# Performance work log

Hardware: AMD Instinct MI355X
Metric: run time of the kernel (lower is better)

Reference implementation:

```python
import jax, jax.numpy as jnp
import numpy as np

B, G, FI, FO, H, W = 16, 8, 64, 64, 64, 64
N_ITER = 3


def setup_inputs() -> dict:
    key = jax.random.key(0)
    kx, kw, kb = jax.random.split(key, 3)
    x = jax.random.normal(kx, (B, G * FI, H, W), dtype=jnp.float32)
    # kaiming_normal_ on [fo*g, fi, 1, 1]: std = sqrt(2 / fan_in), fan_in = fi*1*1
    weight = jax.random.normal(kw, (FO * G, FI, 1, 1), dtype=jnp.float32) * np.sqrt(2.0 / FI)
    bias = jax.random.normal(kb, (1, FO, 1, 1), dtype=jnp.float32) * 0.01
    return {"x": x, "weight": weight, "bias": bias}


def reference(x, weight, bias):
    g, n_iter = G, N_ITER
    gfo, fi = weight.shape[:2]
    fo = gfo // g
    b, c, h, w = x.shape
    # grouped 1x1 conv == per-group channel matmul
    xg = x.reshape(b, g, fi, h, w)
    wg = weight.reshape(g, fo, fi)
    con = jnp.einsum('bgihw,gfi->bgfhw', xg, wg)  # [B, g, fo, H, W]
    beta = jnp.zeros((), dtype=x.dtype)
    for i in range(n_iter):
        alpha = jax.nn.sigmoid(beta)
        v = jnp.sum(alpha * con, axis=1, keepdims=True)  # [B, 1, fo, H, W]
        if i == n_iter - 1:
            out = v[:, 0]  # [B, fo, H, W]
            return out + bias
        beta = beta + jnp.sum(v * con, axis=2, keepdims=True)  # [B, g, 1, H, W]
```

## Files before the change

kernel.cpp:

```cpp
#include <hip/hip_runtime.h>


typedef __attribute__((ext_vector_type(8))) _Float16 half8;
typedef __attribute__((ext_vector_type(4))) float f32x4;

#define NG   8
#define NFI  64
#define NFO  64
#define HW   4096

__device__ __forceinline__ float sigmoidf_fast(float v) {
    float e = __builtin_amdgcn_exp2f(-1.44269504088896f * v);
    return __builtin_amdgcn_rcpf(1.0f + e);
}

__global__ __launch_bounds__(256)
void wconv_kernel(const float* __restrict__ w, _Float16* __restrict__ wbuf) {
    int V = blockIdx.x * 256 + threadIdx.x;
    int g    = V >> 10;
    int t    = (V >> 8) & 3;
    int c    = (V >> 6) & 3;
    int lane = V & 63;
    int pl = lane & 15, q = lane >> 4;
    const float* src = w + g * (NFO * NFI) + (t * 16 + pl) * NFI + (c & 1) * 32 + q * 8;
    half8 o;
    #pragma unroll
    for (int j = 0; j < 8; ++j) {
        float f = src[j];
        _Float16 h = (_Float16)f;
        o[j] = (c >> 1) ? (_Float16)(f - (float)h) : h;
    }
    *(half8*)(wbuf + (size_t)V * 8) = o;
}

__global__ __launch_bounds__(256, 2)
void routing_kernel(const float* __restrict__ x,
                    const _Float16* __restrict__ wbuf,
                    const float* __restrict__ bias,
                    float* __restrict__ out) {
    const int tid  = threadIdx.x;
    const int b    = blockIdx.x >> 6;
    const int p0   = (blockIdx.x & 63) << 6;
    const int lane = tid & 63;
    const int wv   = tid >> 6;
    const int pl   = lane & 15;
    const int q    = lane >> 4;
    const int pw   = wv * 16 + pl;

    const float* xg = x + (size_t)b * (NG * NFI) * HW + p0 + pw;

    f32x4 acc[NG][4];
    #pragma unroll
    for (int g = 0; g < NG; ++g)
        #pragma unroll
        for (int t = 0; t < 4; ++t)
            acc[g][t] = (f32x4){0.f, 0.f, 0.f, 0.f};

#define XDECL(NM) float NM##0, NM##1, NM##2, NM##3, NM##4, NM##5, NM##6, NM##7, \
                        NM##8, NM##9, NM##10, NM##11, NM##12, NM##13, NM##14, NM##15;
#define XLOAD(G, NM)                                                         \
    {                                                                        \
        const float* p_ = xg + (size_t)((G) * 64 + q * 8) * HW;              \
        NM##0 = p_[(size_t)0 * HW];  NM##1 = p_[(size_t)1 * HW];             \
        NM##2 = p_[(size_t)2 * HW];  NM##3 = p_[(size_t)3 * HW];             \
        NM##4 = p_[(size_t)4 * HW];  NM##5 = p_[(size_t)5 * HW];             \
        NM##6 = p_[(size_t)6 * HW];  NM##7 = p_[(size_t)7 * HW];             \
        const float* p2_ = p_ + (size_t)32 * HW;                             \
        NM##8  = p2_[(size_t)0 * HW]; NM##9  = p2_[(size_t)1 * HW];          \
        NM##10 = p2_[(size_t)2 * HW]; NM##11 = p2_[(size_t)3 * HW];          \
        NM##12 = p2_[(size_t)4 * HW]; NM##13 = p2_[(size_t)5 * HW];          \
        NM##14 = p2_[(size_t)6 * HW]; NM##15 = p2_[(size_t)7 * HW];          \
    }
#define XGRP(G, NM)                                                          \
    {                                                                        \
        half8 b0, b1;                                                        \
        b0[0] = (_Float16)NM##0;  b0[1] = (_Float16)NM##1;                   \
        b0[2] = (_Float16)NM##2;  b0[3] = (_Float16)NM##3;                   \
        b0[4] = (_Float16)NM##4;  b0[5] = (_Float16)NM##5;                   \
        b0[6] = (_Float16)NM##6;  b0[7] = (_Float16)NM##7;                   \
        b1[0] = (_Float16)NM##8;  b1[1] = (_Float16)NM##9;                   \
        b1[2] = (_Float16)NM##10; b1[3] = (_Float16)NM##11;                  \
        b1[4] = (_Float16)NM##12; b1[5] = (_Float16)NM##13;                  \
        b1[6] = (_Float16)NM##14; b1[7] = (_Float16)NM##15;                  \
        const _Float16* wg_ = wbuf + (size_t)(G) * 16 * 512 + lane * 8;      \
        _Pragma("unroll")                                                    \
        for (int t = 0; t < 4; ++t) {                                        \
            const _Float16* wp_ = wg_ + (size_t)t * 2048;                    \
            half8 a0h = *(const half8*)(wp_);                                \
            half8 a1h = *(const half8*)(wp_ + 512);                          \
            half8 a0l = *(const half8*)(wp_ + 1024);                         \
            half8 a1l = *(const half8*)(wp_ + 1536);                         \
            acc[G][t] = __builtin_amdgcn_mfma_f32_16x16x32_f16(a0h, b0, acc[G][t], 0, 0, 0); \
            acc[G][t] = __builtin_amdgcn_mfma_f32_16x16x32_f16(a1h, b1, acc[G][t], 0, 0, 0); \
            acc[G][t] = __builtin_amdgcn_mfma_f32_16x16x32_f16(a0l, b0, acc[G][t], 0, 0, 0); \
            acc[G][t] = __builtin_amdgcn_mfma_f32_16x16x32_f16(a1l, b1, acc[G][t], 0, 0, 0); \
        }                                                                    \
    }

    XDECL(X0) XDECL(X1) XDECL(X2)

    XLOAD(0, X0)
    XLOAD(1, X1)
    XLOAD(2, X2) XGRP(0, X0)
    XLOAD(3, X0) XGRP(1, X1)
    XLOAD(4, X1) XGRP(2, X2)
    XLOAD(5, X2) XGRP(3, X0)
    XLOAD(6, X0) XGRP(4, X1)
    XLOAD(7, X1) XGRP(5, X2)
    XGRP(6, X0)
    XGRP(7, X1)

#undef XDECL
#undef XLOAD
#undef XGRP

    float v0[4][4];
    #pragma unroll
    for (int t = 0; t < 4; ++t)
        #pragma unroll
        for (int r = 0; r < 4; ++r) {
            float s = 0.f;
            #pragma unroll
            for (int g = 0; g < NG; ++g) s += acc[g][t][r];
            v0[t][r] = 0.5f * s;
        }

    float beta[NG], alpha[NG];
    #pragma unroll
    for (int g = 0; g < NG; ++g) {
        float s = 0.f;
        #pragma unroll
        for (int t = 0; t < 4; ++t)
            #pragma unroll
            for (int r = 0; r < 4; ++r)
                s += v0[t][r] * acc[g][t][r];
        s += __shfl_xor(s, 16);
        s += __shfl_xor(s, 32);
        beta[g]  = s;
        alpha[g] = sigmoidf_fast(s);
    }

    #pragma unroll
    for (int t = 0; t < 4; ++t)
        #pragma unroll
        for (int r = 0; r < 4; ++r) {
            float s = 0.f;
            #pragma unroll
            for (int g = 0; g < NG; ++g) s += alpha[g] * acc[g][t][r];
            v0[t][r] = s;
        }
    #pragma unroll
    for (int g = 0; g < NG; ++g) {
        float s = 0.f;
        #pragma unroll
        for (int t = 0; t < 4; ++t)
            #pragma unroll
            for (int r = 0; r < 4; ++r)
                s += v0[t][r] * acc[g][t][r];
        s += __shfl_xor(s, 16);
        s += __shfl_xor(s, 32);
        beta[g] += s;
        alpha[g] = sigmoidf_fast(beta[g]);
    }

    #pragma unroll
    for (int t = 0; t < 4; ++t)
        #pragma unroll
        for (int r = 0; r < 4; ++r) {
            int f = t * 16 + q * 4 + r;
            float s = bias[f];
            #pragma unroll
            for (int g = 0; g < NG; ++g) s += alpha[g] * acc[g][t][r];
            out[((size_t)(b * NFO + f)) * HW + p0 + pw] = s;
        }
}

extern "C" void kernel_launch(void* const* d_in, const int* in_sizes, int n_in,
                              void* d_out, int out_size, void* d_ws, size_t ws_size,
                              hipStream_t stream) {
    const float* x    = (const float*)d_in[0];
    const float* w    = (const float*)d_in[1];
    const float* bias = (const float*)d_in[2];
    float* out = (float*)d_out;
    _Float16* wbuf = (_Float16*)d_ws;

    wconv_kernel<<<32, 256, 0, stream>>>(w, wbuf);
    routing_kernel<<<1024, 256, 0, stream>>>(x, wbuf, bias, out);
}
```

Before: 211.6 us.

## Stage per-group weights into LDS with double-buffered async global_load_lds

Instead of every wave reading the fp16 split weight fragments straight from global memory for each group, the block cooperatively copies each group's weights into a double-buffered LDS array using global_load_lds. The copies are interleaved with the x loads, with explicit vmcnt waits and barriers. This is meant to cut redundant global/L2 weight traffic across the four waves and overlap weight fetch with MFMA work. In exchange it adds 32KB of LDS per block, which may limit occupancy, plus block barriers per group and fragile hand-counted waitcnt values.

Result: faster. 206.2 us (-2.5%).

```diff
diff --git a/kernel.cpp b/kernel.cpp
--- a/kernel.cpp
+++ b/kernel.cpp
@@ -47,6 +47,8 @@
     const int q    = lane >> 4;
     const int pw   = wv * 16 + pl;
 
+    __shared__ _Float16 wlds[2][16 * 512];
+
     const float* xg = x + (size_t)b * (NG * NFI) * HW + p0 + pw;
 
     f32x4 acc[NG][4];
@@ -55,6 +57,29 @@
         #pragma unroll
         for (int t = 0; t < 4; ++t)
             acc[g][t] = (f32x4){0.f, 0.f, 0.f, 0.f};
+
+#define CB   asm volatile("" ::: "memory")
+#define BAR  __builtin_amdgcn_s_barrier()
+#define SB0  __builtin_amdgcn_sched_barrier(0)
+#define WAITV(N) asm volatile("s_waitcnt vmcnt(" #N ")" ::: "memory")
+
+#define WSTAGE(G, BUF)                                                        \
+    {                                                                         \
+        const _Float16* ws_ = wbuf + (size_t)(G) * 8192 + (wv * 4) * 512 + lane * 8; \
+        _Float16* wd_ = &wlds[BUF][0] + (wv * 4) * 512;                       \
+        __builtin_amdgcn_global_load_lds(                                     \
+            (const __attribute__((address_space(1))) void*)(ws_),             \
+            (__attribute__((address_space(3))) void*)(wd_), 16, 0, 0);        \
+        __builtin_amdgcn_global_load_lds(                                     \
+            (const __attribute__((address_space(1))) void*)(ws_ + 512),       \
+            (__attribute__((address_space(3))) void*)(wd_ + 512), 16, 0, 0);  \
+        __builtin_amdgcn_global_load_lds(                                     \
+            (const __attribute__((address_space(1))) void*)(ws_ + 1024),      \
+            (__attribute__((address_space(3))) void*)(wd_ + 1024), 16, 0, 0); \
+        __builtin_amdgcn_global_load_lds(                                     \
+            (const __attribute__((address_space(1))) void*)(ws_ + 1536),      \
+            (__attribute__((address_space(3))) void*)(wd_ + 1536), 16, 0, 0); \
+    }
 
 #define XDECL(NM) float NM##0, NM##1, NM##2, NM##3, NM##4, NM##5, NM##6, NM##7, \
                         NM##8, NM##9, NM##10, NM##11, NM##12, NM##13, NM##14, NM##15;
@@ -71,7 +96,7 @@
         NM##12 = p2_[(size_t)4 * HW]; NM##13 = p2_[(size_t)5 * HW];          \
         NM##14 = p2_[(size_t)6 * HW]; NM##15 = p2_[(size_t)7 * HW];          \
     }
-#define XGRP(G, NM)                                                          \
+#define XGRP(G, NM, BUF)                                                     \
     {                                                                        \
         half8 b0, b1;                                                        \
         b0[0] = (_Float16)NM##0;  b0[1] = (_Float16)NM##1;                   \
@@ -82,7 +107,7 @@
         b1[2] = (_Float16)NM##10; b1[3] = (_Float16)NM##11;                  \
         b1[4] = (_Float16)NM##12; b1[5] = (_Float16)NM##13;                  \
         b1[6] = (_Float16)NM##14; b1[7] = (_Float16)NM##15;                  \
-        const _Float16* wg_ = wbuf + (size_t)(G) * 16 * 512 + lane * 8;      \
+        const _Float16* wg_ = &wlds[BUF][0] + lane * 8;                      \
         _Pragma("unroll")                                                    \
         for (int t = 0; t < 4; ++t) {                                        \
             const _Float16* wp_ = wg_ + (size_t)t * 2048;                    \
@@ -99,20 +124,28 @@
 
     XDECL(X0) XDECL(X1) XDECL(X2)
 
-    XLOAD(0, X0)
-    XLOAD(1, X1)
-    XLOAD(2, X2) XGRP(0, X0)
-    XLOAD(3, X0) XGRP(1, X1)
-    XLOAD(4, X1) XGRP(2, X2)
-    XLOAD(5, X2) XGRP(3, X0)
-    XLOAD(6, X0) XGRP(4, X1)
-    XLOAD(7, X1) XGRP(5, X2)
-    XGRP(6, X0)
-    XGRP(7, X1)
+    WSTAGE(0, 0); CB;
+    XLOAD(0, X0); CB;
+    WSTAGE(1, 1); CB;
+    XLOAD(1, X1); CB;
+
+    XLOAD(2, X2); WAITV(36); BAR; SB0; XGRP(0, X0, 0); BAR; WSTAGE(2, 0); CB;
+    XLOAD(3, X0); WAITV(36); BAR; SB0; XGRP(1, X1, 1); BAR; WSTAGE(3, 1); CB;
+    XLOAD(4, X1); WAITV(36); BAR; SB0; XGRP(2, X2, 0); BAR; WSTAGE(4, 0); CB;
+    XLOAD(5, X2); WAITV(36); BAR; SB0; XGRP(3, X0, 1); BAR; WSTAGE(5, 1); CB;
+    XLOAD(6, X0); WAITV(36); BAR; SB0; XGRP(4, X1, 0); BAR; WSTAGE(6, 0); CB;
+    XLOAD(7, X1); WAITV(36); BAR; SB0; XGRP(5, X2, 1); BAR; WSTAGE(7, 1); CB;
+                  WAITV(20); BAR; SB0; XGRP(6, X0, 0);
+                  WAITV(0);  BAR; SB0; XGRP(7, X1, 1);
 
 #undef XDECL
 #undef XLOAD
 #undef XGRP
+#undef WSTAGE
+#undef CB
+#undef BAR
+#undef SB0
+#undef WAITV
 
     float v0[4][4];
     #pragma unroll
```
